# Kernel optimization log

Hardware: AMD Instinct MI355X
Metric: run time of the kernel (lower is better)

Reference implementation:

```python
import jax, jax.numpy as jnp
import numpy as np

B, T = 8, 512
N_QUBITS, N_ROT, D_PER = 64, 16, 64
D = N_QUBITS * D_PER


def setup_inputs() -> dict:
    key = jax.random.key(0)
    k1, k2, k3, k4 = jax.random.split(key, 4)
    return {
        "x": jax.random.normal(k1, (B, T, D), dtype=jnp.float32),
        "rx_params": jax.random.normal(k2, (N_QUBITS, N_ROT), dtype=jnp.float32),
        "ry_params": jax.random.normal(k3, (N_QUBITS, N_ROT), dtype=jnp.float32),
        "rz_params": jax.random.normal(k4, (N_QUBITS, N_ROT), dtype=jnp.float32),
    }


def _rot_diag(theta, axis):
    # theta: (Q,) per-qubit angle. The torch einsum 'btqd,btqq->btqd' only uses
    # the diagonal of the (Q,Q) rotation matrix. For rx/ry, the paired-qubit
    # construction puts cos(theta_k/2) on both diagonal slots of pair k
    # (first Q//2 angles are used, matching cos[..., :len(idx)]).
    Q = theta.shape[0]
    half = theta[: Q // 2] * 0.5
    if axis in ("x", "y"):
        return jnp.repeat(jnp.cos(half).astype(jnp.complex64), 2)
    # rz: diag(exp(-i a/2), exp(+i a/2)) interleaved over pairs
    e = jnp.exp(-1j * half.astype(jnp.complex64))
    return jnp.stack([e, jnp.conj(e)], axis=-1).reshape(-1)


def _apply_rotation(state, theta, axis):
    # state: (B, T, Q, d_per) complex64
    sf = jnp.fft.fft2(state, axes=(-2, -1))
    sf = sf * _rot_diag(theta, axis)[:, None]  # diagonal per-qubit scale
    return jnp.fft.ifft2(sf, axes=(-2, -1)).real  # torch takes .real


def reference(x, rx_params, ry_params, rz_params):
    b, t, d = x.shape
    q = rx_params.shape[0]
    state = x.reshape(b, t, q, d // q).astype(jnp.complex64)
    for params, axis in ((rx_params, "x"), (ry_params, "y"), (rz_params, "z")):
        theta = params.sum(-1)  # combine n_rotations into one angle per qubit
        state = _apply_rotation(state, theta, axis).astype(jnp.complex64)
    state = state.reshape(b, t, d)
    # noise model: (1 + amp_noise) * exp(i * phase_noise) * state, then L2 norm
    ka, kp = jax.random.split(jax.random.key(42))
    amp = 0.01 * jax.random.normal(ka, state.shape, dtype=jnp.float32)
    ph = 0.005 * jax.random.normal(kp, state.shape, dtype=jnp.float32)
    noisy = (1.0 + amp) * jnp.exp(1j * ph.astype(jnp.complex64)) * state
    norm = jnp.linalg.norm(noisy, axis=-1, keepdims=True)
    noisy = noisy / (norm + 1e-8)
    return jnp.abs(noisy)  # measurement
```

## Files before the change

### kernel.cpp

```cpp
#include <hip/hip_runtime.h>
#include <stdint.h>

typedef _Float16 half8 __attribute__((ext_vector_type(8)));
typedef float floatx4 __attribute__((ext_vector_type(4)));

__device__ __forceinline__ uint32_t rotl32(uint32_t v, int r) {
  return (v << r) | (v >> (32 - r));
}

__device__ __forceinline__ void threefry2x32(uint32_t k0, uint32_t k1,
                                             uint32_t x0, uint32_t x1,
                                             uint32_t& o0, uint32_t& o1) {
  uint32_t k2 = k0 ^ k1 ^ 0x1BD11BDAu;
  x0 += k0; x1 += k1;
#define TF_R(r) { x0 += x1; x1 = rotl32(x1, (r)); x1 ^= x0; }
  TF_R(13) TF_R(15) TF_R(26) TF_R(6)   x0 += k1; x1 += k2 + 1u;
  TF_R(17) TF_R(29) TF_R(16) TF_R(24)  x0 += k2; x1 += k0 + 2u;
  TF_R(13) TF_R(15) TF_R(26) TF_R(6)   x0 += k0; x1 += k1 + 3u;
  TF_R(17) TF_R(29) TF_R(16) TF_R(24)  x0 += k1; x1 += k2 + 4u;
  TF_R(13) TF_R(15) TF_R(26) TF_R(6)   x0 += k2; x1 += k0 + 5u;
#undef TF_R
  o0 = x0; o1 = x1;
}

__device__ __forceinline__ float erfinv_fast(float x) {
  float w = -__logf(fmaf(-x, x, 1.0f));
  float p;
  if (__builtin_expect(w >= 5.0f, 0)) {
    w = sqrtf(w) - 3.0f;
    p = -0.000200214257f;
    p = fmaf(p, w, 0.000100950558f);
    p = fmaf(p, w, 0.00134934322f);
    p = fmaf(p, w, -0.00367342844f);
    p = fmaf(p, w, 0.00573950773f);
    p = fmaf(p, w, -0.0076224613f);
    p = fmaf(p, w, 0.00943887047f);
    p = fmaf(p, w, 1.00167406f);
    p = fmaf(p, w, 2.83297682f);
  } else {
    w = w - 2.5f;
    p = 2.81022636e-08f;
    p = fmaf(p, w, 3.43273939e-07f);
    p = fmaf(p, w, -3.5233877e-06f);
    p = fmaf(p, w, -4.39150654e-06f);
    p = fmaf(p, w, 0.00021858087f);
    p = fmaf(p, w, -0.00125372503f);
    p = fmaf(p, w, -0.00417768164f);
    p = fmaf(p, w, 0.246640727f);
    p = fmaf(p, w, 1.50140941f);
  }
  return p * x;
}

__device__ __align__(16) _Float16 g_afrag[256 * 16];
__device__ uint32_t g_key[2];

__global__ void setup_kernel(const float* __restrict__ rx,
                             const float* __restrict__ ry,
                             const float* __restrict__ rz) {
  __shared__ float cre[3][64], cim[3][64];
  __shared__ float Gr[64], Gi[64];
  __shared__ float twc[64], tws[64];
  __shared__ float gs[64];
  const int t = threadIdx.x;

  if (t < 32) {
    const float* ps[3] = {rx, ry, rz};
    for (int a = 0; a < 3; ++a) {
      float s = 0.0f;
      for (int r = 0; r < 16; ++r) s += ps[a][t * 16 + r];
      float h = 0.5f * s;
      float ch = cosf(h), sh = sinf(h);
      if (a < 2) {
        cre[a][2 * t] = ch;     cim[a][2 * t] = 0.0f;
        cre[a][2 * t + 1] = ch; cim[a][2 * t + 1] = 0.0f;
      } else {
        cre[2][2 * t] = ch;     cim[2][2 * t] = -sh;
        cre[2][2 * t + 1] = ch; cim[2][2 * t + 1] = sh;
      }
    }
  }
  if (t < 64) {
    double ang = (2.0 * 3.14159265358979323846 / 64.0) * (double)t;
    twc[t] = (float)cos(ang);
    tws[t] = (float)sin(ang);
  }
  __syncthreads();

  if (t < 64) {
    const int k = t, kn = (64 - k) & 63;
    float pr = 1.0f, pi = 0.0f;
    for (int a = 0; a < 3; ++a) {
      float cr = 0.5f * (cre[a][k] + cre[a][kn]);
      float ci = 0.5f * (cim[a][k] - cim[a][kn]);
      float nr = pr * cr - pi * ci;
      float ni = pr * ci + pi * cr;
      pr = nr; pi = ni;
    }
    Gr[k] = pr; Gi[k] = pi;
  }
  __syncthreads();

  if (t < 64) {
    const int mi = t;
    float s = 0.0f;
    for (int k = 0; k < 64; ++k) {
      int idx = (k * mi) & 63;
      s = fmaf(Gr[k], twc[idx], s);
      s = fmaf(-Gi[k], tws[idx], s);
    }
    gs[mi] = s * (1.0f / 64.0f);
  }
  __syncthreads();

  {
    const int w = t >> 6, lane = t & 63, quad = lane >> 4, m = lane & 15;
    const int r0 = 16 * w + m - 8 * quad;
#pragma unroll
    for (int j = 0; j < 8; ++j) {
      g_afrag[t * 16 + j]     = (_Float16)gs[(r0 - j) & 63];
      g_afrag[t * 16 + 8 + j] = (_Float16)gs[(r0 - 32 - j) & 63];
    }
  }

  if (t == 0) {
    uint32_t o0, o1;
    threefry2x32(0u, 42u, 0u, 0u, o0, o1);
    g_key[0] = o0; g_key[1] = o1;
  }
}

__global__ __launch_bounds__(256, 8) void qmain(const float* __restrict__ x,
                                                float* __restrict__ out) {
  __shared__ __align__(16) _Float16 Xt[64 * 72];
  __shared__ float red[4];
  const int tid = threadIdx.x;
  const int row = blockIdx.x;
  const int lane = tid & 63;
  const int w = tid >> 6;
  const int quad = lane >> 4;
  const int m = lane & 15;

  const half8* at = (const half8*)g_afrag;
  half8 af0 = at[2 * tid];
  half8 af1 = at[2 * tid + 1];
  const uint32_t ka0 = g_key[0], ka1 = g_key[1];

  {
    const float* xr = x + (size_t)row * 4096;
    const int d0 = (tid & 31) * 2;
    const int q0 = (tid >> 5) * 8;
    float2 v[8];
#pragma unroll
    for (int s = 0; s < 8; ++s) v[s] = *(const float2*)(xr + (q0 + s) * 64 + d0);
    union { _Float16 h[8]; uint4 u; } r0, r1;
#pragma unroll
    for (int s = 0; s < 8; ++s) { r0.h[s] = (_Float16)v[s].x; r1.h[s] = (_Float16)v[s].y; }
    *(uint4*)&Xt[d0 * 72 + q0] = r0.u;
    *(uint4*)&Xt[(d0 + 1) * 72 + q0] = r1.u;
  }
  __syncthreads();

  floatx4 acc[4];
#pragma unroll
  for (int c = 0; c < 4; ++c) {
    const _Float16* bp = &Xt[(16 * c + m) * 72 + 8 * quad];
    half8 b0 = *(const half8*)bp;
    half8 b1 = *(const half8*)(bp + 32);
    acc[c] = (floatx4){0.0f, 0.0f, 0.0f, 0.0f};
    acc[c] = __builtin_amdgcn_mfma_f32_16x16x32_f16(af0, b0, acc[c], 0, 0, 0);
    acc[c] = __builtin_amdgcn_mfma_f32_16x16x32_f16(af1, b1, acc[c], 0, 0, 0);
  }

  const uint32_t idxbase = ((uint32_t)row << 12) + (uint32_t)(((16 * w + 4 * quad) << 6) + m);
  float wv[16];
  float ssum = 0.0f;
#pragma unroll
  for (int c = 0; c < 4; ++c) {
#pragma unroll
    for (int r = 0; r < 4; ++r) {
      const uint32_t idx = idxbase + (uint32_t)(r * 64 + 16 * c);
      uint32_t o0, o1;
      threefry2x32(ka0, ka1, 0u, idx, o0, o1);
      uint32_t bits = o0 ^ o1;
      float vf = __uint_as_float((bits >> 9) | 0x3f800000u);
      float u = fmaxf(fmaf(vf, 2.0f, -3.0f), -0.99999994f);
      float val = fmaf(erfinv_fast(u), 0.014142135623730951f, 1.0f) * acc[c][r];
      ssum = fmaf(val, val, ssum);
      wv[c * 4 + r] = val;
    }
  }

#pragma unroll
  for (int off = 32; off >= 1; off >>= 1) ssum += __shfl_xor(ssum, off, 64);
  if (lane == 0) red[w] = ssum;
  __syncthreads();
  const float total = red[0] + red[1] + red[2] + red[3];
  const float scale = 1.0f / (sqrtf(total) + 1e-8f);

  float* ob = out + (size_t)row * 4096 + (size_t)(((16 * w + 4 * quad) << 6) + m);
#pragma unroll
  for (int c = 0; c < 4; ++c)
#pragma unroll
    for (int r = 0; r < 4; ++r)
      ob[r * 64 + 16 * c] = fabsf(wv[c * 4 + r]) * scale;
}

extern "C" void kernel_launch(void* const* d_in, const int* in_sizes, int n_in,
                              void* d_out, int out_size, void* d_ws, size_t ws_size,
                              hipStream_t stream) {
  const float* x  = (const float*)d_in[0];
  const float* rx = (const float*)d_in[1];
  const float* ry = (const float*)d_in[2];
  const float* rz = (const float*)d_in[3];
  float* out = (float*)d_out;

  setup_kernel<<<1, 256, 0, stream>>>(rx, ry, rz);
  qmain<<<4096, 256, 0, stream>>>(x, out);
}
```

Before: 143.3 us.

## Overlap noise generation with global loads and trim erfinv polynomial

Moves the threefry/erfinv noise computation ahead of the MFMA stage, split around the LDS transpose, so it can hide the latency of the global x loads. Uses alignbit for rotates and mantissa packing, and log2 instead of log. Truncates the central-branch erfinv polynomial from 9 to 5 terms, which lowers ALU work but reduces the accuracy of the noise values. It also keeps 16 extra registers live across the load phase, which may affect occupancy.

Result: faster. 135.2 us (-5.7%).

```diff
diff --git a/kernel.cpp b/kernel.cpp
--- a/kernel.cpp
+++ b/kernel.cpp
@@ -5,7 +5,7 @@
 typedef float floatx4 __attribute__((ext_vector_type(4)));
 
 __device__ __forceinline__ uint32_t rotl32(uint32_t v, int r) {
-  return (v << r) | (v >> (32 - r));
+  return __builtin_amdgcn_alignbit(v, v, 32 - r);
 }
 
 __device__ __forceinline__ void threefry2x32(uint32_t k0, uint32_t k1,
@@ -23,33 +23,37 @@
   o0 = x0; o1 = x1;
 }
 
-__device__ __forceinline__ float erfinv_fast(float x) {
-  float w = -__logf(fmaf(-x, x, 1.0f));
+__device__ __forceinline__ float noise_mult(uint32_t ka0, uint32_t ka1,
+                                            uint32_t idx) {
+  uint32_t o0, o1;
+  threefry2x32(ka0, ka1, 0u, idx, o0, o1);
+  uint32_t bits = o0 ^ o1;
+  float vf = __uint_as_float(__builtin_amdgcn_alignbit(0x7Fu, bits, 9));
+  float u = fmaxf(fmaf(vf, 2.0f, -3.0f), -0.99999994f);
+  float t = fmaf(-u, u, 1.0f);
+  float l2 = __log2f(t);
   float p;
-  if (__builtin_expect(w >= 5.0f, 0)) {
-    w = sqrtf(w) - 3.0f;
+  if (__builtin_expect(l2 <= -7.2134752f, 0)) {
+    float w = l2 * -0.69314718f;
+    float s = sqrtf(w) - 3.0f;
     p = -0.000200214257f;
-    p = fmaf(p, w, 0.000100950558f);
-    p = fmaf(p, w, 0.00134934322f);
-    p = fmaf(p, w, -0.00367342844f);
-    p = fmaf(p, w, 0.00573950773f);
-    p = fmaf(p, w, -0.0076224613f);
-    p = fmaf(p, w, 0.00943887047f);
-    p = fmaf(p, w, 1.00167406f);
-    p = fmaf(p, w, 2.83297682f);
+    p = fmaf(p, s, 0.000100950558f);
+    p = fmaf(p, s, 0.00134934322f);
+    p = fmaf(p, s, -0.00367342844f);
+    p = fmaf(p, s, 0.00573950773f);
+    p = fmaf(p, s, -0.0076224613f);
+    p = fmaf(p, s, 0.00943887047f);
+    p = fmaf(p, s, 1.00167406f);
+    p = fmaf(p, s, 2.83297682f);
   } else {
-    w = w - 2.5f;
-    p = 2.81022636e-08f;
-    p = fmaf(p, w, 3.43273939e-07f);
-    p = fmaf(p, w, -3.5233877e-06f);
-    p = fmaf(p, w, -4.39150654e-06f);
-    p = fmaf(p, w, 0.00021858087f);
-    p = fmaf(p, w, -0.00125372503f);
-    p = fmaf(p, w, -0.00417768164f);
-    p = fmaf(p, w, 0.246640727f);
-    p = fmaf(p, w, 1.50140941f);
-  }
-  return p * x;
+    float a = fmaf(l2, -0.69314718f, -2.5f);
+    p = 0.00021858087f;
+    p = fmaf(p, a, -0.00125372503f);
+    p = fmaf(p, a, -0.00417768164f);
+    p = fmaf(p, a, 0.246640727f);
+    p = fmaf(p, a, 1.50140941f);
+  }
+  return fmaf(p, u * 0.014142135623730951f, 1.0f);
 }
 
 __device__ __align__(16) _Float16 g_afrag[256 * 16];
@@ -141,24 +145,42 @@
   const int quad = lane >> 4;
   const int m = lane & 15;
 
+  const float* xr = x + (size_t)row * 4096;
+  const int d0 = (tid & 31) * 2;
+  const int q0 = (tid >> 5) * 8;
+  float2 v[8];
+#pragma unroll
+  for (int s = 0; s < 8; ++s) v[s] = *(const float2*)(xr + (q0 + s) * 64 + d0);
+
+  const uint32_t ka0 = g_key[0], ka1 = g_key[1];
+  const uint32_t idxbase = ((uint32_t)row << 12) +
+                           (uint32_t)(((16 * w + 4 * quad) << 6) + m);
+
+  float nm[16];
+#pragma unroll
+  for (int c = 0; c < 2; ++c)
+#pragma unroll
+    for (int r = 0; r < 4; ++r)
+      nm[c * 4 + r] = noise_mult(ka0, ka1, idxbase + (uint32_t)(r * 64 + 16 * c));
+
+  {
+    union { _Float16 h[8]; uint4 u; } r0, r1;
+#pragma unroll
+    for (int s = 0; s < 8; ++s) { r0.h[s] = (_Float16)v[s].x; r1.h[s] = (_Float16)v[s].y; }
+    *(uint4*)&Xt[d0 * 72 + q0] = r0.u;
+    *(uint4*)&Xt[(d0 + 1) * 72 + q0] = r1.u;
+  }
+
   const half8* at = (const half8*)g_afrag;
   half8 af0 = at[2 * tid];
   half8 af1 = at[2 * tid + 1];
-  const uint32_t ka0 = g_key[0], ka1 = g_key[1];
-
-  {
-    const float* xr = x + (size_t)row * 4096;
-    const int d0 = (tid & 31) * 2;
-    const int q0 = (tid >> 5) * 8;
-    float2 v[8];
-#pragma unroll
-    for (int s = 0; s < 8; ++s) v[s] = *(const float2*)(xr + (q0 + s) * 64 + d0);
-    union { _Float16 h[8]; uint4 u; } r0, r1;
-#pragma unroll
-    for (int s = 0; s < 8; ++s) { r0.h[s] = (_Float16)v[s].x; r1.h[s] = (_Float16)v[s].y; }
-    *(uint4*)&Xt[d0 * 72 + q0] = r0.u;
-    *(uint4*)&Xt[(d0 + 1) * 72 + q0] = r1.u;
-  }
+
+#pragma unroll
+  for (int c = 2; c < 4; ++c)
+#pragma unroll
+    for (int r = 0; r < 4; ++r)
+      nm[c * 4 + r] = noise_mult(ka0, ka1, idxbase + (uint32_t)(r * 64 + 16 * c));
+
   __syncthreads();
 
   floatx4 acc[4];
@@ -172,20 +194,13 @@
     acc[c] = __builtin_amdgcn_mfma_f32_16x16x32_f16(af1, b1, acc[c], 0, 0, 0);
   }
 
-  const uint32_t idxbase = ((uint32_t)row << 12) + (uint32_t)(((16 * w + 4 * quad) << 6) + m);
   float wv[16];
   float ssum = 0.0f;
 #pragma unroll
   for (int c = 0; c < 4; ++c) {
 #pragma unroll
     for (int r = 0; r < 4; ++r) {
-      const uint32_t idx = idxbase + (uint32_t)(r * 64 + 16 * c);
-      uint32_t o0, o1;
-      threefry2x32(ka0, ka1, 0u, idx, o0, o1);
-      uint32_t bits = o0 ^ o1;
-      float vf = __uint_as_float((bits >> 9) | 0x3f800000u);
-      float u = fmaxf(fmaf(vf, 2.0f, -3.0f), -0.99999994f);
-      float val = fmaf(erfinv_fast(u), 0.014142135623730951f, 1.0f) * acc[c][r];
+      float val = nm[c * 4 + r] * acc[c][r];
       ssum = fmaf(val, val, ssum);
       wv[c * 4 + r] = val;
     }
```
